# Kernel tuning notes

Measured on AMD Instinct MI355X. Metric: run time of the kernel, lower is better.

Reference implementation:

```python
import jax, jax.numpy as jnp
import numpy as np

N_NODES = 50000
N_EDGES = 800000
N_TRAIN = 40000
IN_DIM = 129  # node_dim + encoding_dim


def _gatv2(x, src, dst, Wl, Wr, att, bias, heads, out_ch, n_nodes):
    """PyG GATv2Conv (share_weights=False, concat=True, aggr='mean', eval mode).
    x: [N, F_in]; src/dst: [E]; Wl/Wr: [F_in, heads*out_ch]; att: [heads, out_ch]."""
    xl = (x @ Wl).reshape(-1, heads, out_ch)          # source transform  [N,H,C]
    xr = (x @ Wr).reshape(-1, heads, out_ch)          # target transform  [N,H,C]
    e = jax.nn.leaky_relu(xl[src] + xr[dst], 0.2)     # [E,H,C]
    logits = jnp.einsum('ehc,hc->eh', e, att)         # [E,H]
    # segment softmax over incoming edges of each target node
    m = jax.ops.segment_max(logits, dst, num_segments=n_nodes)   # [N,H]
    a = jnp.exp(logits - m[dst])
    denom = jax.ops.segment_sum(a, dst, num_segments=n_nodes)    # [N,H]
    alpha = a / denom[dst]                                       # [E,H]
    msg = xl[src] * alpha[:, :, None]                            # [E,H,C]
    summed = jax.ops.segment_sum(msg, dst, num_segments=n_nodes) # [N,H,C]
    deg = jax.ops.segment_sum(jnp.ones((src.shape[0],), x.dtype), dst,
                              num_segments=n_nodes)              # aggr='mean'
    out = summed / jnp.maximum(deg, 1.0)[:, None, None]
    return out.reshape(n_nodes, heads * out_ch) + bias


def setup_inputs() -> dict:
    key = jax.random.key(0)
    ks = jax.random.split(key, 16)
    x = jax.random.normal(ks[0], (N_NODES, IN_DIM), jnp.float32)
    edge_index = jax.random.randint(ks[1], (2, N_EDGES), 0, N_NODES, jnp.int64)
    y = jax.random.uniform(ks[2], (N_NODES,), jnp.float32)
    train_idx = jnp.sort(jax.random.randint(ks[3], (N_TRAIN,), 0, N_NODES, jnp.int64))

    def lin(k, fi, fo):
        return jax.random.normal(k, (fi, fo), jnp.float32) * (1.0 / np.sqrt(fi))

    return {
        'x': x, 'edge_index': edge_index, 'y': y, 'train_idx': train_idx,
        # layer 1: 129 -> 128, heads=2 (concat -> 256)
        'W1l': lin(ks[4], IN_DIM, 256), 'W1r': lin(ks[5], IN_DIM, 256),
        'a1': jax.random.normal(ks[6], (2, 128), jnp.float32) * 0.1,
        'b1': jnp.zeros((256,), jnp.float32),
        # layer 2: 256 -> 128, heads=1
        'W2l': lin(ks[7], 256, 128), 'W2r': lin(ks[8], 256, 128),
        'a2': jax.random.normal(ks[9], (1, 128), jnp.float32) * 0.1,
        'b2': jnp.zeros((128,), jnp.float32),
        # layer 3: 128 -> 1, heads=1
        'W3l': lin(ks[10], 128, 1), 'W3r': lin(ks[11], 128, 1),
        'a3': jax.random.normal(ks[12], (1, 1), jnp.float32) * 0.1,
        'b3': jnp.zeros((1,), jnp.float32),
    }


def reference(x, edge_index, y, train_idx,
              W1l, W1r, a1, b1, W2l, W2r, a2, b2, W3l, W3r, a3, b3):
    src, dst = edge_index[0], edge_index[1]
    n = x.shape[0]
    h = _gatv2(x, src, dst, W1l, W1r, a1, b1, 2, 128, n)   # [N,256]
    h = _gatv2(h, src, dst, W2l, W2r, a2, b2, 1, 128, n)   # [N,128]
    h = _gatv2(h, src, dst, W3l, W3r, a3, b3, 1, 1, n)     # [N,1]
    pred = jax.nn.sigmoid(h.squeeze(-1))                   # [N]
    return pred[train_idx], y[train_idx]
```

## Files before the change

### kernel.cpp

```cpp
#include <hip/hip_runtime.h>
#include <cmath>

__device__ __forceinline__ float lo16(unsigned u){ union{unsigned x; float f;} c; c.x = u << 16; return c.f; }
__device__ __forceinline__ float hi16(unsigned u){ union{unsigned x; float f;} c; c.x = u & 0xffff0000u; return c.f; }
__device__ __forceinline__ float leaky(float v){ return fmaxf(v, 0.2f*v); }
__device__ __forceinline__ unsigned short f2bf(float f){
  union { float f; unsigned u; } c; c.f = f;
  unsigned u = c.u + 0x7FFFu + ((c.u >> 16) & 1u);
  return (unsigned short)(u >> 16);
}
__device__ __forceinline__ unsigned pack2bf(float a, float b){
  return (unsigned)f2bf(a) | ((unsigned)f2bf(b) << 16);
}
__device__ __forceinline__ float mergef(float m, float M){ return (m == M) ? 1.f : __expf(m - M); }

typedef __attribute__((ext_vector_type(8))) short bfrag;
typedef __attribute__((ext_vector_type(4))) float ffrag;


__global__ void deg_kernel(const int* __restrict__ dst, int* __restrict__ degi, int E){
  int e = blockIdx.x*256 + threadIdx.x;
  if (e < E) atomicAdd(&degi[dst[e]], 1);
}

__global__ void scan_p1(const int* __restrict__ degi, int* __restrict__ bsum, int N){
  __shared__ int red[256];
  int t = threadIdx.x;
  int i = blockIdx.x*256 + t;
  red[t] = (i < N) ? degi[i] : 0;
  __syncthreads();
  for (int off = 128; off > 0; off >>= 1){
    if (t < off) red[t] += red[t + off];
    __syncthreads();
  }
  if (t == 0) bsum[blockIdx.x] = red[0];
}

__global__ void scan_p2(const int* __restrict__ bsum, int* __restrict__ boff,
                        int* __restrict__ row_off, int NB, int N){
  __shared__ int s[256];
  int t = threadIdx.x;
  int v = (t < NB) ? bsum[t] : 0;
  s[t] = v;
  __syncthreads();
  for (int off = 1; off < 256; off <<= 1){
    int q = (t >= off) ? s[t - off] : 0;
    __syncthreads();
    s[t] += q;
    __syncthreads();
  }
  if (t < NB) boff[t] = s[t] - v;
  if (t == NB-1) row_off[N] = s[t];
}

__global__ void scan_p3(const int* __restrict__ degi, const int* __restrict__ boff,
                        int* __restrict__ row_off, int N){
  __shared__ int s[256];
  int t = threadIdx.x;
  int i = blockIdx.x*256 + t;
  int v = (i < N) ? degi[i] : 0;
  s[t] = v;
  __syncthreads();
  for (int off = 1; off < 256; off <<= 1){
    int q = (t >= off) ? s[t - off] : 0;
    __syncthreads();
    s[t] += q;
    __syncthreads();
  }
  if (i < N) row_off[i] = boff[blockIdx.x] + s[t] - v;
}

__global__ void scatter_kernel(const int* __restrict__ src, const int* __restrict__ dst,
                               const int* __restrict__ row_off, int* __restrict__ cursor,
                               int* __restrict__ csr_src, int E){
  int e = blockIdx.x*256 + threadIdx.x;
  if (e < E){
    int d = dst[e];
    int pos = row_off[d] + atomicAdd(&cursor[d], 1);
    csr_src[pos] = src[e];
  }
}


__global__ void prep_all(const float* __restrict__ x,
                         const float* __restrict__ W1l, const float* __restrict__ W1r,
                         const float* __restrict__ W2l, const float* __restrict__ W2r,
                         unsigned short* __restrict__ Xbf,
                         unsigned short* __restrict__ WT1,
                         unsigned short* __restrict__ WT2, int N){
  int idx = blockIdx.x*256 + threadIdx.x;
  int n1 = N*160;
  int n2 = 2*256*160;
  int n3 = 2*128*256;
  if (idx < n1){
    int n = idx / 160, k = idx - n*160;
    Xbf[idx] = (k < 129) ? f2bf(x[(size_t)n*129 + k]) : (unsigned short)0;
  } else if (idx < n1 + n2){
    int j = idx - n1;
    int c = j / 160, k = j - c*160;
    float v = 0.f;
    if (k < 129) v = (c < 256) ? W1l[(size_t)k*256 + c] : W1r[(size_t)k*256 + (c - 256)];
    WT1[j] = f2bf(v);
  } else if (idx < n1 + n2 + n3){
    int j = idx - n1 - n2;
    int c = j >> 8, k = j & 255;
    float v = (c < 128) ? W2l[(size_t)k*128 + c] : W2r[(size_t)k*128 + (c - 128)];
    WT2[j] = f2bf(v);
  }
}


template<int CB>
__global__ __launch_bounds__(256) void gemm_dual(const unsigned short* __restrict__ Xbf,
                                                 const unsigned short* __restrict__ WT,
                                                 unsigned short* __restrict__ outL,
                                                 unsigned short* __restrict__ outR,
                                                 int N, int Kpad, int Mhalf){
  __shared__ __attribute__((aligned(16))) unsigned short Xs[128*40];
  __shared__ __attribute__((aligned(16))) unsigned short Ws[CB*128*40];
  int t = threadIdx.x;
  int n0 = blockIdx.x*128, c0 = blockIdx.y*(CB*128);
  int wv = t >> 6, lane = t & 63;
  int wr = wv >> 1, wc = wv & 1;
  int m16 = lane & 15, quad = lane >> 4;

  ffrag acc[CB][4][4];
  #pragma unroll
  for (int cb = 0; cb < CB; cb++)
    #pragma unroll
    for (int i = 0; i < 4; i++)
      #pragma unroll
      for (int j = 0; j < 4; j++) acc[cb][i][j] = (ffrag){0.f,0.f,0.f,0.f};

  for (int k0 = 0; k0 < Kpad; k0 += 32){
    uint4 zero = {0,0,0,0};
    #pragma unroll
    for (int it = 0; it < 2; it++){
      int idx = t + it*256;
      int r = idx >> 2, g = idx & 3;
      int n = n0 + r;
      uint4 v = (n < N) ? *(const uint4*)&Xbf[(size_t)n*Kpad + k0 + g*8] : zero;
      *(uint4*)&Xs[r*40 + g*8] = v;
    }
    #pragma unroll
    for (int it = 0; it < 2*CB; it++){
      int idx = t + it*256;
      int c = idx >> 2, g = idx & 3;
      uint4 v = *(const uint4*)&WT[(size_t)(c0 + c)*Kpad + k0 + g*8];
      *(uint4*)&Ws[c*40 + g*8] = v;
    }
    __syncthreads();
    bfrag a[4];
    #pragma unroll
    for (int i = 0; i < 4; i++)
      a[i] = *(const bfrag*)&Xs[(wr*64 + i*16 + m16)*40 + quad*8];
    #pragma unroll
    for (int cb = 0; cb < CB; cb++){
      bfrag b[4];
      #pragma unroll
      for (int j = 0; j < 4; j++)
        b[j] = *(const bfrag*)&Ws[(cb*128 + wc*64 + j*16 + m16)*40 + quad*8];
      #pragma unroll
      for (int i = 0; i < 4; i++)
        #pragma unroll
        for (int j = 0; j < 4; j++)
          acc[cb][i][j] = __builtin_amdgcn_mfma_f32_16x16x32_bf16(a[i], b[j], acc[cb][i][j], 0, 0, 0);
    }
    __syncthreads();
  }

  #pragma unroll
  for (int cb = 0; cb < CB; cb++){
    int gc0 = c0 + cb*128;
    bool isL = (gc0 < Mhalf);
    unsigned short* outp = isL ? outL : outR;
    int ccol0 = isL ? gc0 : (gc0 - Mhalf);
    #pragma unroll
    for (int i = 0; i < 4; i++){
      #pragma unroll
      for (int reg = 0; reg < 4; reg++){
        int rr = n0 + wr*64 + i*16 + quad*4 + reg;
        if (rr >= N) continue;
        #pragma unroll
        for (int j = 0; j < 4; j++){
          int cc = ccol0 + wc*64 + j*16 + m16;
          outp[(size_t)rr*Mhalf + cc] = f2bf(acc[cb][i][j][reg]);
        }
      }
    }
  }
}


__global__ __launch_bounds__(256) void fused_gat_wave2(
    const int* __restrict__ row_off, const int* __restrict__ csr_src,
    const unsigned short* __restrict__ xlbf, const unsigned short* __restrict__ xrbf,
    const float* __restrict__ att, const float* __restrict__ bias,
    unsigned short* __restrict__ outbf, int N)
{
  int n = blockIdx.x*4 + (threadIdx.x >> 6);
  if (n >= N) return;
  int lane = threadIdx.x & 63;
  int slot = lane >> 5;
  int sub  = lane & 31;
  int ch0  = sub*8;
  int r0 = row_off[n], r1 = row_off[n+1];
  int deg = r1 - r0;

  uint4 xru = *(const uint4*)&xrbf[(size_t)n*256 + ch0];
  float q0=lo16(xru.x), q1=hi16(xru.x), q2=lo16(xru.y), q3=hi16(xru.y);
  float q4=lo16(xru.z), q5=hi16(xru.z), q6=lo16(xru.w), q7=hi16(xru.w);
  const float4* atp = (const float4*)(att + ch0);
  float4 ata = atp[0], atb = atp[1];

  float m = -INFINITY, l = 0.f;
  float a0=0.f,a1=0.f,a2=0.f,a3=0.f,a4=0.f,a5=0.f,a6=0.f,a7=0.f;

  if (deg > 0){
    int p = r0 + slot;
    int pc = min(p, r1-1);
    uint4 cur = *(const uint4*)&xlbf[(size_t)csr_src[pc]*256 + ch0];
    for (; p < r1; p += 2){
      int pn = min(p+2, r1-1);
      uint4 nxt = *(const uint4*)&xlbf[(size_t)csr_src[pn]*256 + ch0];
      float x0=lo16(cur.x), x1=hi16(cur.x), x2=lo16(cur.y), x3=hi16(cur.y);
      float x4=lo16(cur.z), x5=hi16(cur.z), x6=lo16(cur.w), x7=hi16(cur.w);
      float dot = leaky(x0+q0)*ata.x + leaky(x1+q1)*ata.y
                + leaky(x2+q2)*ata.z + leaky(x3+q3)*ata.w
                + leaky(x4+q4)*atb.x + leaky(x5+q5)*atb.y
                + leaky(x6+q6)*atb.z + leaky(x7+q7)*atb.w;
      dot += __shfl_xor(dot, 8);
      dot += __shfl_xor(dot, 4);
      dot += __shfl_xor(dot, 2);
      dot += __shfl_xor(dot, 1);
      if (dot <= m){
        float w_ = __expf(dot - m);
        l += w_;
        a0 += w_*x0; a1 += w_*x1; a2 += w_*x2; a3 += w_*x3;
        a4 += w_*x4; a5 += w_*x5; a6 += w_*x6; a7 += w_*x7;
      } else {
        float sc = __expf(m - dot);
        l = l*sc + 1.f;
        a0 = a0*sc + x0; a1 = a1*sc + x1; a2 = a2*sc + x2; a3 = a3*sc + x3;
        a4 = a4*sc + x4; a5 = a5*sc + x5; a6 = a6*sc + x6; a7 = a7*sc + x7;
        m = dot;
      }
      cur = nxt;
    }
  }

  const float4* bvp = (const float4*)(bias + ch0);
  float4 res0 = bvp[0], res1 = bvp[1];
  if (deg > 0){
    float m2 = __shfl_xor(m, 32);
    float l2 = __shfl_xor(l, 32);
    float M  = fmaxf(m, m2);
    float fa = mergef(m, M), fb = mergef(m2, M);
    float L  = l*fa + l2*fb;
    float q;
    q = __shfl_xor(a0,32); a0 = a0*fa + q*fb;
    q = __shfl_xor(a1,32); a1 = a1*fa + q*fb;
    q = __shfl_xor(a2,32); a2 = a2*fa + q*fb;
    q = __shfl_xor(a3,32); a3 = a3*fa + q*fb;
    q = __shfl_xor(a4,32); a4 = a4*fa + q*fb;
    q = __shfl_xor(a5,32); a5 = a5*fa + q*fb;
    q = __shfl_xor(a6,32); a6 = a6*fa + q*fb;
    q = __shfl_xor(a7,32); a7 = a7*fa + q*fb;
    float inv = 1.f / (L * (float)deg);
    res0.x += a0*inv; res0.y += a1*inv; res0.z += a2*inv; res0.w += a3*inv;
    res1.x += a4*inv; res1.y += a5*inv; res1.z += a6*inv; res1.w += a7*inv;
  }
  if (slot == 0){
    uint4 u;
    u.x = pack2bf(res0.x, res0.y);
    u.y = pack2bf(res0.z, res0.w);
    u.z = pack2bf(res1.x, res1.y);
    u.w = pack2bf(res1.z, res1.w);
    *(uint4*)&outbf[(size_t)n*256 + ch0] = u;
  }
}


__global__ __launch_bounds__(256) void fused_gat_wave1(
    const int* __restrict__ row_off, const int* __restrict__ csr_src,
    const unsigned short* __restrict__ xlbf, const unsigned short* __restrict__ xrbf,
    const float* __restrict__ att, const float* __restrict__ bias,
    unsigned short* __restrict__ outbf, int N)
{
  int n = blockIdx.x*4 + (threadIdx.x >> 6);
  if (n >= N) return;
  int lane = threadIdx.x & 63;
  int slot = lane >> 4;
  int sub  = lane & 15;
  int ch0  = sub*8;
  int r0 = row_off[n], r1 = row_off[n+1];
  int deg = r1 - r0;

  uint4 xru = *(const uint4*)&xrbf[(size_t)n*128 + ch0];
  float q0=lo16(xru.x), q1=hi16(xru.x), q2=lo16(xru.y), q3=hi16(xru.y);
  float q4=lo16(xru.z), q5=hi16(xru.z), q6=lo16(xru.w), q7=hi16(xru.w);
  const float4* atp = (const float4*)(att + ch0);
  float4 ata = atp[0], atb = atp[1];

  float m = -INFINITY, l = 0.f;
  float a0=0.f,a1=0.f,a2=0.f,a3=0.f,a4=0.f,a5=0.f,a6=0.f,a7=0.f;

  if (deg > 0){
    int p = r0 + slot;
    int pc = min(p, r1-1);
    uint4 cur = *(const uint4*)&xlbf[(size_t)csr_src[pc]*128 + ch0];
    for (; p < r1; p += 4){
      int pn = min(p+4, r1-1);
      uint4 nxt = *(const uint4*)&xlbf[(size_t)csr_src[pn]*128 + ch0];
      float x0=lo16(cur.x), x1=hi16(cur.x), x2=lo16(cur.y), x3=hi16(cur.y);
      float x4=lo16(cur.z), x5=hi16(cur.z), x6=lo16(cur.w), x7=hi16(cur.w);
      float dot = leaky(x0+q0)*ata.x + leaky(x1+q1)*ata.y
                + leaky(x2+q2)*ata.z + leaky(x3+q3)*ata.w
                + leaky(x4+q4)*atb.x + leaky(x5+q5)*atb.y
                + leaky(x6+q6)*atb.z + leaky(x7+q7)*atb.w;
      dot += __shfl_xor(dot, 8);
      dot += __shfl_xor(dot, 4);
      dot += __shfl_xor(dot, 2);
      dot += __shfl_xor(dot, 1);
      if (dot <= m){
        float w_ = __expf(dot - m);
        l += w_;
        a0 += w_*x0; a1 += w_*x1; a2 += w_*x2; a3 += w_*x3;
        a4 += w_*x4; a5 += w_*x5; a6 += w_*x6; a7 += w_*x7;
      } else {
        float sc = __expf(m - dot);
        l = l*sc + 1.f;
        a0 = a0*sc + x0; a1 = a1*sc + x1; a2 = a2*sc + x2; a3 = a3*sc + x3;
        a4 = a4*sc + x4; a5 = a5*sc + x5; a6 = a6*sc + x6; a7 = a7*sc + x7;
        m = dot;
      }
      cur = nxt;
    }
  }

  const float4* bvp = (const float4*)(bias + ch0);
  float4 res0 = bvp[0], res1 = bvp[1];
  if (deg > 0){
    #pragma unroll
    for (int stage = 0; stage < 2; stage++){
      int d = 16 << stage;
      float m2 = __shfl_xor(m, d);
      float l2 = __shfl_xor(l, d);
      float M  = fmaxf(m, m2);
      float fa = mergef(m, M), fb = mergef(m2, M);
      l = l*fa + l2*fb;
      float q;
      q = __shfl_xor(a0,d); a0 = a0*fa + q*fb;
      q = __shfl_xor(a1,d); a1 = a1*fa + q*fb;
      q = __shfl_xor(a2,d); a2 = a2*fa + q*fb;
      q = __shfl_xor(a3,d); a3 = a3*fa + q*fb;
      q = __shfl_xor(a4,d); a4 = a4*fa + q*fb;
      q = __shfl_xor(a5,d); a5 = a5*fa + q*fb;
      q = __shfl_xor(a6,d); a6 = a6*fa + q*fb;
      q = __shfl_xor(a7,d); a7 = a7*fa + q*fb;
      m = M;
    }
    float inv = 1.f / (l * (float)deg);
    res0.x += a0*inv; res0.y += a1*inv; res0.z += a2*inv; res0.w += a3*inv;
    res1.x += a4*inv; res1.y += a5*inv; res1.z += a6*inv; res1.w += a7*inv;
  }
  if (slot == 0){
    uint4 u;
    u.x = pack2bf(res0.x, res0.y);
    u.y = pack2bf(res0.z, res0.w);
    u.z = pack2bf(res1.x, res1.y);
    u.w = pack2bf(res1.z, res1.w);
    *(uint4*)&outbf[(size_t)n*128 + ch0] = u;
  }
}


__global__ __launch_bounds__(256) void gemm3_kernel(const unsigned short* __restrict__ h2,
                                                    const float* __restrict__ W3l,
                                                    const float* __restrict__ W3r,
                                                    float* __restrict__ xl3,
                                                    float* __restrict__ xr3, int N){
  int n = blockIdx.x*4 + (threadIdx.x >> 6);
  int lane = threadIdx.x & 63;
  if (n >= N) return;
  unsigned u = *(const unsigned*)&h2[(size_t)n*128 + lane*2];
  float v1 = lo16(u), v2 = hi16(u);
  float al = v1*W3l[lane*2] + v2*W3l[lane*2+1];
  float ar = v1*W3r[lane*2] + v2*W3r[lane*2+1];
  #pragma unroll
  for (int off = 32; off > 0; off >>= 1){
    al += __shfl_xor(al, off);
    ar += __shfl_xor(ar, off);
  }
  if (lane == 0){ xl3[n] = al; xr3[n] = ar; }
}

__global__ __launch_bounds__(256) void aggr3_wave(
    const int* __restrict__ row_off, const int* __restrict__ csr_src,
    const float* __restrict__ xl3, const float* __restrict__ xr3,
    const float* __restrict__ a3, const float* __restrict__ b3,
    float* __restrict__ h3, int N)
{
  int n = blockIdx.x*4 + (threadIdx.x >> 6);
  if (n >= N) return;
  int lane = threadIdx.x & 63;
  int r0 = row_off[n], r1 = row_off[n+1];
  int deg = r1 - r0;
  float b = b3[0];
  if (deg == 0){ if (lane == 0) h3[n] = b; return; }
  float xrv = xr3[n];
  float aa = a3[0];
  float m = -INFINITY, den = 0.f, s = 0.f;
  for (int base = r0; base < r1; base += 64){
    int p = base + lane;
    bool valid = p < r1;
    float xlv = valid ? xl3[csr_src[p]] : 0.f;
    float t = xlv + xrv;
    float v = fmaxf(t, 0.2f*t) * aa;
    if (!valid) v = -INFINITY;
    float bm = v;
    #pragma unroll
    for (int off = 32; off > 0; off >>= 1) bm = fmaxf(bm, __shfl_xor(bm, off));
    float nm = fmaxf(m, bm);
    float a = valid ? __expf(v - nm) : 0.f;
    float bd = a, bs = a * xlv;
    #pragma unroll
    for (int off = 32; off > 0; off >>= 1){
      bd += __shfl_xor(bd, off);
      bs += __shfl_xor(bs, off);
    }
    float sc = __expf(m - nm);
    den = den*sc + bd;
    s   = s*sc + bs;
    m = nm;
  }
  if (lane == 0) h3[n] = s/den/(float)deg + b;
}

__global__ void out_kernel(const float* __restrict__ h3, const float* __restrict__ y,
                           const int* __restrict__ tidx, float* __restrict__ out, int T){
  int i = blockIdx.x*256 + threadIdx.x;
  if (i >= T) return;
  int n = tidx[i];
  out[i] = 1.f/(1.f + __expf(-h3[n]));
  out[T + i] = y[n];
}


extern "C" void kernel_launch(void* const* d_in, const int* in_sizes, int n_in,
                              void* d_out, int out_size, void* d_ws, size_t ws_size,
                              hipStream_t stream){
  const float* x    = (const float*)d_in[0];
  const int*   ei   = (const int*)d_in[1];
  const float* y    = (const float*)d_in[2];
  const int*   tidx = (const int*)d_in[3];
  const float* W1l  = (const float*)d_in[4];
  const float* W1r  = (const float*)d_in[5];
  const float* a1   = (const float*)d_in[6];
  const float* b1   = (const float*)d_in[7];
  const float* W2l  = (const float*)d_in[8];
  const float* W2r  = (const float*)d_in[9];
  const float* a2   = (const float*)d_in[10];
  const float* b2   = (const float*)d_in[11];
  const float* W3l  = (const float*)d_in[12];
  const float* W3r  = (const float*)d_in[13];
  const float* a3   = (const float*)d_in[14];
  const float* b3   = (const float*)d_in[15];

  int N = in_sizes[2];
  int E = in_sizes[1] / 2;
  int T = in_sizes[3];
  const int* src = ei;
  const int* dst = ei + E;
  int NB = (N + 255) / 256;

  char* w = (char*)d_ws;
  size_t off = 0;
  auto take = [&](size_t bytes) -> char* {
    char* p = w + off;
    off = (off + bytes + 255) & ~(size_t)255;
    return p;
  };
  int*   row_off = (int*)  take((size_t)(N+1)*4);
  int*   degi    = (int*)  take((size_t)N*4);
  int*   cursor  = (int*)  take((size_t)N*4);
  int*   bsum    = (int*)  take((size_t)NB*4);
  int*   boff    = (int*)  take((size_t)NB*4);
  int*   csr_src = (int*)  take((size_t)E*4);
  unsigned short* WT1 = (unsigned short*)take((size_t)512*160*2);
  unsigned short* WT2 = (unsigned short*)take((size_t)256*256*2);
  float* A       = (float*)take((size_t)N*256*4);
  float* B       = (float*)take((size_t)N*256*4);

  hipMemsetAsync(degi, 0, (size_t)N*4, stream);
  hipMemsetAsync(cursor, 0, (size_t)N*4, stream);
  deg_kernel<<<(E+255)/256, 256, 0, stream>>>(dst, degi, E);
  scan_p1<<<NB, 256, 0, stream>>>(degi, bsum, N);
  scan_p2<<<1, 256, 0, stream>>>(bsum, boff, row_off, NB, N);
  scan_p3<<<NB, 256, 0, stream>>>(degi, boff, row_off, N);
  scatter_kernel<<<(E+255)/256, 256, 0, stream>>>(src, dst, row_off, cursor, csr_src, E);

  unsigned short* xl1bf = (unsigned short*)A;
  unsigned short* Xbf   = (unsigned short*)(A + (size_t)N*128);
  unsigned short* h1bf  = (unsigned short*)(A + (size_t)N*128);
  unsigned short* xr1bf = (unsigned short*)B;
  float* Bu   = B + (size_t)N*128;
  float* xl3  = Bu;
  float* xr3  = Bu + N;
  float* h3   = Bu + 2*(size_t)N;

  int prep_total = N*160 + 2*256*160 + 2*128*256;
  prep_all<<<(prep_total+255)/256, 256, 0, stream>>>(x, W1l, W1r, W2l, W2r, Xbf, WT1, WT2, N);

  gemm_dual<2><<<dim3((N+127)/128, 2), 256, 0, stream>>>(Xbf, WT1, xl1bf, xr1bf, N, 160, 256);
  fused_gat_wave2<<<(N+3)/4, 256, 0, stream>>>(row_off, csr_src, xl1bf, xr1bf, a1, b1, h1bf, N);

  unsigned short* xl2bf = (unsigned short*)A;
  unsigned short* xr2bf = (unsigned short*)B;
  gemm_dual<2><<<dim3((N+127)/128, 1), 256, 0, stream>>>(h1bf, WT2, xl2bf, xr2bf, N, 256, 128);
  fused_gat_wave1<<<(N+3)/4, 256, 0, stream>>>(row_off, csr_src, xl2bf, xr2bf, a2, b2, xr2bf, N);
  unsigned short* h2bf = xr2bf;

  gemm3_kernel<<<(N+3)/4, 256, 0, stream>>>(h2bf, W3l, W3r, xl3, xr3, N);
  aggr3_wave<<<(N+3)/4, 256, 0, stream>>>(row_off, csr_src, xl3, xr3, a3, b3, h3, N);

  out_kernel<<<(T+255)/256, 256, 0, stream>>>(h3, y, tidx, (float*)d_out, T);
}
```

Baseline: 394.8 us.

## Fuse layer-3 projection into layer-2 aggregation and streamline attention math

Folds the layer-3 linear projection (gemm3) into the layer-2 fused GAT kernel, so h2 is never written out or read back. The cursor memset is dropped by having the scan seed the scatter cursors with the row offsets directly. The attention inner loops are rewritten: leaky ReLU becomes 0.6*t + 0.4*|t| with log2e pre-folded into the coefficients so exp2f replaces __expf, and the min-clamped edge prefetch is replaced by reads padded past the end of csr_src. These cut launches, memory traffic and per-edge ALU work. In exchange the prefetch reads one row beyond each node's range and relies on four padding entries at the end of csr_src.

New measurement: 419.8 us. +6.3%, slower.

```diff
diff --git a/kernel.cpp b/kernel.cpp
--- a/kernel.cpp
+++ b/kernel.cpp
@@ -3,7 +3,6 @@
 
 __device__ __forceinline__ float lo16(unsigned u){ union{unsigned x; float f;} c; c.x = u << 16; return c.f; }
 __device__ __forceinline__ float hi16(unsigned u){ union{unsigned x; float f;} c; c.x = u & 0xffff0000u; return c.f; }
-__device__ __forceinline__ float leaky(float v){ return fmaxf(v, 0.2f*v); }
 __device__ __forceinline__ unsigned short f2bf(float f){
   union { float f; unsigned u; } c; c.f = f;
   unsigned u = c.u + 0x7FFFu + ((c.u >> 16) & 1u);
@@ -12,7 +11,9 @@
 __device__ __forceinline__ unsigned pack2bf(float a, float b){
   return (unsigned)f2bf(a) | ((unsigned)f2bf(b) << 16);
 }
-__device__ __forceinline__ float mergef(float m, float M){ return (m == M) ? 1.f : __expf(m - M); }
+__device__ __forceinline__ float mergef2(float m, float M){ return (m == M) ? 1.f : exp2f(m - M); }
+
+#define LOG2E 1.4426950408889634f
 
 typedef __attribute__((ext_vector_type(8))) short bfrag;
 typedef __attribute__((ext_vector_type(4))) float ffrag;
@@ -54,7 +55,7 @@
 }
 
 __global__ void scan_p3(const int* __restrict__ degi, const int* __restrict__ boff,
-                        int* __restrict__ row_off, int N){
+                        int* __restrict__ row_off, int* __restrict__ cur, int N){
   __shared__ int s[256];
   int t = threadIdx.x;
   int i = blockIdx.x*256 + t;
@@ -67,17 +68,21 @@
     s[t] += q;
     __syncthreads();
   }
-  if (i < N) row_off[i] = boff[blockIdx.x] + s[t] - v;
+  if (i < N){
+    int ro = boff[blockIdx.x] + s[t] - v;
+    row_off[i] = ro;
+    cur[i] = ro;
+  }
 }
 
 __global__ void scatter_kernel(const int* __restrict__ src, const int* __restrict__ dst,
-                               const int* __restrict__ row_off, int* __restrict__ cursor,
-                               int* __restrict__ csr_src, int E){
+                               int* __restrict__ cur, int* __restrict__ csr_src, int E){
   int e = blockIdx.x*256 + threadIdx.x;
   if (e < E){
-    int d = dst[e];
-    int pos = row_off[d] + atomicAdd(&cursor[d], 1);
+    int pos = atomicAdd(&cur[dst[e]], 1);
     csr_src[pos] = src[e];
+  } else if (e < E + 4){
+    csr_src[e] = 0;
   }
 }
 
@@ -211,52 +216,60 @@
   float q0=lo16(xru.x), q1=hi16(xru.x), q2=lo16(xru.y), q3=hi16(xru.y);
   float q4=lo16(xru.z), q5=hi16(xru.z), q6=lo16(xru.w), q7=hi16(xru.w);
   const float4* atp = (const float4*)(att + ch0);
-  float4 ata = atp[0], atb = atp[1];
+  float4 aa = atp[0], ab = atp[1];
+  float4 p6a, p6b, p4a, p4b;
+  p6a.x=0.6f*LOG2E*aa.x; p6a.y=0.6f*LOG2E*aa.y; p6a.z=0.6f*LOG2E*aa.z; p6a.w=0.6f*LOG2E*aa.w;
+  p6b.x=0.6f*LOG2E*ab.x; p6b.y=0.6f*LOG2E*ab.y; p6b.z=0.6f*LOG2E*ab.z; p6b.w=0.6f*LOG2E*ab.w;
+  p4a.x=0.4f*LOG2E*aa.x; p4a.y=0.4f*LOG2E*aa.y; p4a.z=0.4f*LOG2E*aa.z; p4a.w=0.4f*LOG2E*aa.w;
+  p4b.x=0.4f*LOG2E*ab.x; p4b.y=0.4f*LOG2E*ab.y; p4b.z=0.4f*LOG2E*ab.z; p4b.w=0.4f*LOG2E*ab.w;
 
   float m = -INFINITY, l = 0.f;
   float a0=0.f,a1=0.f,a2=0.f,a3=0.f,a4=0.f,a5=0.f,a6=0.f,a7=0.f;
 
-  if (deg > 0){
-    int p = r0 + slot;
-    int pc = min(p, r1-1);
-    uint4 cur = *(const uint4*)&xlbf[(size_t)csr_src[pc]*256 + ch0];
-    for (; p < r1; p += 2){
-      int pn = min(p+2, r1-1);
-      uint4 nxt = *(const uint4*)&xlbf[(size_t)csr_src[pn]*256 + ch0];
-      float x0=lo16(cur.x), x1=hi16(cur.x), x2=lo16(cur.y), x3=hi16(cur.y);
-      float x4=lo16(cur.z), x5=hi16(cur.z), x6=lo16(cur.w), x7=hi16(cur.w);
-      float dot = leaky(x0+q0)*ata.x + leaky(x1+q1)*ata.y
-                + leaky(x2+q2)*ata.z + leaky(x3+q3)*ata.w
-                + leaky(x4+q4)*atb.x + leaky(x5+q5)*atb.y
-                + leaky(x6+q6)*atb.z + leaky(x7+q7)*atb.w;
-      dot += __shfl_xor(dot, 8);
-      dot += __shfl_xor(dot, 4);
-      dot += __shfl_xor(dot, 2);
-      dot += __shfl_xor(dot, 1);
-      if (dot <= m){
-        float w_ = __expf(dot - m);
-        l += w_;
-        a0 += w_*x0; a1 += w_*x1; a2 += w_*x2; a3 += w_*x3;
-        a4 += w_*x4; a5 += w_*x5; a6 += w_*x6; a7 += w_*x7;
-      } else {
-        float sc = __expf(m - dot);
-        l = l*sc + 1.f;
-        a0 = a0*sc + x0; a1 = a1*sc + x1; a2 = a2*sc + x2; a3 = a3*sc + x3;
-        a4 = a4*sc + x4; a5 = a5*sc + x5; a6 = a6*sc + x6; a7 = a7*sc + x7;
-        m = dot;
-      }
-      cur = nxt;
-    }
-  }
-
-  const float4* bvp = (const float4*)(bias + ch0);
-  float4 res0 = bvp[0], res1 = bvp[1];
-  if (deg > 0){
+  const char* xlb = (const char*)xlbf;
+  unsigned chb = (unsigned)ch0*2;
+  int p = r0 + slot;
+  unsigned off0 = ((unsigned)csr_src[p] << 9) + chb;
+  uint4 cur = *(const uint4*)(xlb + off0);
+  for (; p < r1; p += 2){
+    unsigned offn = ((unsigned)csr_src[p+2] << 9) + chb;
+    uint4 nxt = *(const uint4*)(xlb + offn);
+    float x0=lo16(cur.x), x1=hi16(cur.x), x2=lo16(cur.y), x3=hi16(cur.y);
+    float x4=lo16(cur.z), x5=hi16(cur.z), x6=lo16(cur.w), x7=hi16(cur.w);
+    float t0=x0+q0, t1=x1+q1, t2=x2+q2, t3=x3+q3;
+    float t4=x4+q4, t5=x5+q5, t6=x6+q6, t7=x7+q7;
+    float s6 = p6a.x*t0;
+    s6 = fmaf(p6a.y,t1,s6); s6 = fmaf(p6a.z,t2,s6); s6 = fmaf(p6a.w,t3,s6);
+    s6 = fmaf(p6b.x,t4,s6); s6 = fmaf(p6b.y,t5,s6); s6 = fmaf(p6b.z,t6,s6); s6 = fmaf(p6b.w,t7,s6);
+    float s4 = p4a.x*fabsf(t0);
+    s4 = fmaf(p4a.y,fabsf(t1),s4); s4 = fmaf(p4a.z,fabsf(t2),s4); s4 = fmaf(p4a.w,fabsf(t3),s4);
+    s4 = fmaf(p4b.x,fabsf(t4),s4); s4 = fmaf(p4b.y,fabsf(t5),s4); s4 = fmaf(p4b.z,fabsf(t6),s4); s4 = fmaf(p4b.w,fabsf(t7),s4);
+    float dot = s6 + s4;
+    dot += __shfl_xor(dot, 8);
+    dot += __shfl_xor(dot, 4);
+    dot += __shfl_xor(dot, 2);
+    dot += __shfl_xor(dot, 1);
+    if (dot <= m){
+      float w_ = exp2f(dot - m);
+      l += w_;
+      a0 += w_*x0; a1 += w_*x1; a2 += w_*x2; a3 += w_*x3;
+      a4 += w_*x4; a5 += w_*x5; a6 += w_*x6; a7 += w_*x7;
+    } else {
+      float sc = exp2f(m - dot);
+      l = l*sc + 1.f;
+      a0 = a0*sc + x0; a1 = a1*sc + x1; a2 = a2*sc + x2; a3 = a3*sc + x3;
+      a4 = a4*sc + x4; a5 = a5*sc + x5; a6 = a6*sc + x6; a7 = a7*sc + x7;
+      m = dot;
+    }
+    cur = nxt;
+  }
+
+  {
     float m2 = __shfl_xor(m, 32);
     float l2 = __shfl_xor(l, 32);
     float M  = fmaxf(m, m2);
-    float fa = mergef(m, M), fb = mergef(m2, M);
-    float L  = l*fa + l2*fb;
+    float fa = mergef2(m, M), fb = mergef2(m2, M);
+    l = l*fa + l2*fb;
     float q;
     q = __shfl_xor(a0,32); a0 = a0*fa + q*fb;
     q = __shfl_xor(a1,32); a1 = a1*fa + q*fb;
@@ -266,10 +279,12 @@
     q = __shfl_xor(a5,32); a5 = a5*fa + q*fb;
     q = __shfl_xor(a6,32); a6 = a6*fa + q*fb;
     q = __shfl_xor(a7,32); a7 = a7*fa + q*fb;
-    float inv = 1.f / (L * (float)deg);
-    res0.x += a0*inv; res0.y += a1*inv; res0.z += a2*inv; res0.w += a3*inv;
-    res1.x += a4*inv; res1.y += a5*inv; res1.z += a6*inv; res1.w += a7*inv;
-  }
+  }
+  float inv = (deg > 0) ? 1.f/(l*(float)deg) : 0.f;
+  const float4* bvp = (const float4*)(bias + ch0);
+  float4 res0 = bvp[0], res1 = bvp[1];
+  res0.x += a0*inv; res0.y += a1*inv; res0.z += a2*inv; res0.w += a3*inv;
+  res1.x += a4*inv; res1.y += a5*inv; res1.z += a6*inv; res1.w += a7*inv;
   if (slot == 0){
     uint4 u;
     u.x = pack2bf(res0.x, res0.y);
@@ -285,13 +300,14 @@
     const int* __restrict__ row_off, const int* __restrict__ csr_src,
     const unsigned short* __restrict__ xlbf, const unsigned short* __restrict__ xrbf,
     const float* __restrict__ att, const float* __restrict__ bias,
-    unsigned short* __restrict__ outbf, int N)
+    const float* __restrict__ W3l, const float* __restrict__ W3r,
+    float* __restrict__ xl3, float* __restrict__ xr3, int N)
 {
   int n = blockIdx.x*4 + (threadIdx.x >> 6);
   if (n >= N) return;
   int lane = threadIdx.x & 63;
+  int sub  = lane & 15;
   int slot = lane >> 4;
-  int sub  = lane & 15;
   int ch0  = sub*8;
   int r0 = row_off[n], r1 = row_off[n+1];
   int deg = r1 - r0;
@@ -300,100 +316,92 @@
   float q0=lo16(xru.x), q1=hi16(xru.x), q2=lo16(xru.y), q3=hi16(xru.y);
   float q4=lo16(xru.z), q5=hi16(xru.z), q6=lo16(xru.w), q7=hi16(xru.w);
   const float4* atp = (const float4*)(att + ch0);
-  float4 ata = atp[0], atb = atp[1];
+  float4 aa = atp[0], ab = atp[1];
+  float4 p6a, p6b, p4a, p4b;
+  p6a.x=0.6f*LOG2E*aa.x; p6a.y=0.6f*LOG2E*aa.y; p6a.z=0.6f*LOG2E*aa.z; p6a.w=0.6f*LOG2E*aa.w;
+  p6b.x=0.6f*LOG2E*ab.x; p6b.y=0.6f*LOG2E*ab.y; p6b.z=0.6f*LOG2E*ab.z; p6b.w=0.6f*LOG2E*ab.w;
+  p4a.x=0.4f*LOG2E*aa.x; p4a.y=0.4f*LOG2E*aa.y; p4a.z=0.4f*LOG2E*aa.z; p4a.w=0.4f*LOG2E*aa.w;
+  p4b.x=0.4f*LOG2E*ab.x; p4b.y=0.4f*LOG2E*ab.y; p4b.z=0.4f*LOG2E*ab.z; p4b.w=0.4f*LOG2E*ab.w;
 
   float m = -INFINITY, l = 0.f;
   float a0=0.f,a1=0.f,a2=0.f,a3=0.f,a4=0.f,a5=0.f,a6=0.f,a7=0.f;
 
-  if (deg > 0){
-    int p = r0 + slot;
-    int pc = min(p, r1-1);
-    uint4 cur = *(const uint4*)&xlbf[(size_t)csr_src[pc]*128 + ch0];
-    for (; p < r1; p += 4){
-      int pn = min(p+4, r1-1);
-      uint4 nxt = *(const uint4*)&xlbf[(size_t)csr_src[pn]*128 + ch0];
-      float x0=lo16(cur.x), x1=hi16(cur.x), x2=lo16(cur.y), x3=hi16(cur.y);
-      float x4=lo16(cur.z), x5=hi16(cur.z), x6=lo16(cur.w), x7=hi16(cur.w);
-      float dot = leaky(x0+q0)*ata.x + leaky(x1+q1)*ata.y
-                + leaky(x2+q2)*ata.z + leaky(x3+q3)*ata.w
-                + leaky(x4+q4)*atb.x + leaky(x5+q5)*atb.y
-                + leaky(x6+q6)*atb.z + leaky(x7+q7)*atb.w;
-      dot += __shfl_xor(dot, 8);
-      dot += __shfl_xor(dot, 4);
-      dot += __shfl_xor(dot, 2);
-      dot += __shfl_xor(dot, 1);
-      if (dot <= m){
-        float w_ = __expf(dot - m);
-        l += w_;
-        a0 += w_*x0; a1 += w_*x1; a2 += w_*x2; a3 += w_*x3;
-        a4 += w_*x4; a5 += w_*x5; a6 += w_*x6; a7 += w_*x7;
-      } else {
-        float sc = __expf(m - dot);
-        l = l*sc + 1.f;
-        a0 = a0*sc + x0; a1 = a1*sc + x1; a2 = a2*sc + x2; a3 = a3*sc + x3;
-        a4 = a4*sc + x4; a5 = a5*sc + x5; a6 = a6*sc + x6; a7 = a7*sc + x7;
-        m = dot;
-      }
-      cur = nxt;
-    }
-  }
-
+  const char* xlb = (const char*)xlbf;
+  unsigned chb = (unsigned)ch0*2;
+  int p = r0 + slot;
+  unsigned off0 = ((unsigned)csr_src[p] << 8) + chb;
+  uint4 cur = *(const uint4*)(xlb + off0);
+  for (; p < r1; p += 4){
+    unsigned offn = ((unsigned)csr_src[p+4] << 8) + chb;
+    uint4 nxt = *(const uint4*)(xlb + offn);
+    float x0=lo16(cur.x), x1=hi16(cur.x), x2=lo16(cur.y), x3=hi16(cur.y);
+    float x4=lo16(cur.z), x5=hi16(cur.z), x6=lo16(cur.w), x7=hi16(cur.w);
+    float t0=x0+q0, t1=x1+q1, t2=x2+q2, t3=x3+q3;
+    float t4=x4+q4, t5=x5+q5, t6=x6+q6, t7=x7+q7;
+    float s6 = p6a.x*t0;
+    s6 = fmaf(p6a.y,t1,s6); s6 = fmaf(p6a.z,t2,s6); s6 = fmaf(p6a.w,t3,s6);
+    s6 = fmaf(p6b.x,t4,s6); s6 = fmaf(p6b.y,t5,s6); s6 = fmaf(p6b.z,t6,s6); s6 = fmaf(p6b.w,t7,s6);
+    float s4 = p4a.x*fabsf(t0);
+    s4 = fmaf(p4a.y,fabsf(t1),s4); s4 = fmaf(p4a.z,fabsf(t2),s4); s4 = fmaf(p4a.w,fabsf(t3),s4);
+    s4 = fmaf(p4b.x,fabsf(t4),s4); s4 = fmaf(p4b.y,fabsf(t5),s4); s4 = fmaf(p4b.z,fabsf(t6),s4); s4 = fmaf(p4b.w,fabsf(t7),s4);
+    float dot = s6 + s4;
+    dot += __shfl_xor(dot, 8);
+    dot += __shfl_xor(dot, 4);
+    dot += __shfl_xor(dot, 2);
+    dot += __shfl_xor(dot, 1);
+    if (dot <= m){
+      float w_ = exp2f(dot - m);
+      l += w_;
+      a0 += w_*x0; a1 += w_*x1; a2 += w_*x2; a3 += w_*x3;
+      a4 += w_*x4; a5 += w_*x5; a6 += w_*x6; a7 += w_*x7;
+    } else {
+      float sc = exp2f(m - dot);
+      l = l*sc + 1.f;
+      a0 = a0*sc + x0; a1 = a1*sc + x1; a2 = a2*sc + x2; a3 = a3*sc + x3;
+      a4 = a4*sc + x4; a5 = a5*sc + x5; a6 = a6*sc + x6; a7 = a7*sc + x7;
+      m = dot;
+    }
+    cur = nxt;
+  }
+
+  #pragma unroll
+  for (int stage = 0; stage < 2; stage++){
+    int d = 16 << stage;
+    float m2 = __shfl_xor(m, d);
+    float l2 = __shfl_xor(l, d);
+    float M  = fmaxf(m, m2);
+    float fa = mergef2(m, M), fb = mergef2(m2, M);
+    l = l*fa + l2*fb;
+    float q;
+    q = __shfl_xor(a0,d); a0 = a0*fa + q*fb;
+    q = __shfl_xor(a1,d); a1 = a1*fa + q*fb;
+    q = __shfl_xor(a2,d); a2 = a2*fa + q*fb;
+    q = __shfl_xor(a3,d); a3 = a3*fa + q*fb;
+    q = __shfl_xor(a4,d); a4 = a4*fa + q*fb;
+    q = __shfl_xor(a5,d); a5 = a5*fa + q*fb;
+    q = __shfl_xor(a6,d); a6 = a6*fa + q*fb;
+    q = __shfl_xor(a7,d); a7 = a7*fa + q*fb;
+    m = M;
+  }
+  float inv = (deg > 0) ? 1.f/(l*(float)deg) : 0.f;
   const float4* bvp = (const float4*)(bias + ch0);
   float4 res0 = bvp[0], res1 = bvp[1];
-  if (deg > 0){
-    #pragma unroll
-    for (int stage = 0; stage < 2; stage++){
-      int d = 16 << stage;
-      float m2 = __shfl_xor(m, d);
-      float l2 = __shfl_xor(l, d);
-      float M  = fmaxf(m, m2);
-      float fa = mergef(m, M), fb = mergef(m2, M);
-      l = l*fa + l2*fb;
-      float q;
-      q = __shfl_xor(a0,d); a0 = a0*fa + q*fb;
-      q = __shfl_xor(a1,d); a1 = a1*fa + q*fb;
-      q = __shfl_xor(a2,d); a2 = a2*fa + q*fb;
-      q = __shfl_xor(a3,d); a3 = a3*fa + q*fb;
-      q = __shfl_xor(a4,d); a4 = a4*fa + q*fb;
-      q = __shfl_xor(a5,d); a5 = a5*fa + q*fb;
-      q = __shfl_xor(a6,d); a6 = a6*fa + q*fb;
-      q = __shfl_xor(a7,d); a7 = a7*fa + q*fb;
-      m = M;
-    }
-    float inv = 1.f / (l * (float)deg);
-    res0.x += a0*inv; res0.y += a1*inv; res0.z += a2*inv; res0.w += a3*inv;
-    res1.x += a4*inv; res1.y += a5*inv; res1.z += a6*inv; res1.w += a7*inv;
-  }
-  if (slot == 0){
-    uint4 u;
-    u.x = pack2bf(res0.x, res0.y);
-    u.y = pack2bf(res0.z, res0.w);
-    u.z = pack2bf(res1.x, res1.y);
-    u.w = pack2bf(res1.z, res1.w);
-    *(uint4*)&outbf[(size_t)n*128 + ch0] = u;
-  }
-}
-
-
-__global__ __launch_bounds__(256) void gemm3_kernel(const unsigned short* __restrict__ h2,
-                                                    const float* __restrict__ W3l,
-                                                    const float* __restrict__ W3r,
-                                                    float* __restrict__ xl3,
-                                                    float* __restrict__ xr3, int N){
-  int n = blockIdx.x*4 + (threadIdx.x >> 6);
-  int lane = threadIdx.x & 63;
-  if (n >= N) return;
-  unsigned u = *(const unsigned*)&h2[(size_t)n*128 + lane*2];
-  float v1 = lo16(u), v2 = hi16(u);
-  float al = v1*W3l[lane*2] + v2*W3l[lane*2+1];
-  float ar = v1*W3r[lane*2] + v2*W3r[lane*2+1];
-  #pragma unroll
-  for (int off = 32; off > 0; off >>= 1){
-    al += __shfl_xor(al, off);
-    ar += __shfl_xor(ar, off);
-  }
-  if (lane == 0){ xl3[n] = al; xr3[n] = ar; }
-}
+  res0.x += a0*inv; res0.y += a1*inv; res0.z += a2*inv; res0.w += a3*inv;
+  res1.x += a4*inv; res1.y += a5*inv; res1.z += a6*inv; res1.w += a7*inv;
+
+  float4 wla = *(const float4*)(W3l + ch0);
+  float4 wlb = *(const float4*)(W3l + ch0 + 4);
+  float4 wra = *(const float4*)(W3r + ch0);
+  float4 wrb = *(const float4*)(W3r + ch0 + 4);
+  float sl = res0.x*wla.x + res0.y*wla.y + res0.z*wla.z + res0.w*wla.w
+           + res1.x*wlb.x + res1.y*wlb.y + res1.z*wlb.z + res1.w*wlb.w;
+  float sr = res0.x*wra.x + res0.y*wra.y + res0.z*wra.z + res0.w*wra.w
+           + res1.x*wrb.x + res1.y*wrb.y + res1.z*wrb.z + res1.w*wrb.w;
+  sl += __shfl_xor(sl, 8); sl += __shfl_xor(sl, 4); sl += __shfl_xor(sl, 2); sl += __shfl_xor(sl, 1);
+  sr += __shfl_xor(sr, 8); sr += __shfl_xor(sr, 4); sr += __shfl_xor(sr, 2); sr += __shfl_xor(sr, 1);
+  if (lane == 0){ xl3[n] = sl; xr3[n] = sr; }
+}
+
 
 __global__ __launch_bounds__(256) void aggr3_wave(
     const int* __restrict__ row_off, const int* __restrict__ csr_src,
@@ -409,7 +417,7 @@
   float b = b3[0];
   if (deg == 0){ if (lane == 0) h3[n] = b; return; }
   float xrv = xr3[n];
-  float aa = a3[0];
+  float aa = a3[0] * LOG2E;
   float m = -INFINITY, den = 0.f, s = 0.f;
   for (int base = r0; base < r1; base += 64){
     int p = base + lane;
@@ -422,14 +430,14 @@
     #pragma unroll
     for (int off = 32; off > 0; off >>= 1) bm = fmaxf(bm, __shfl_xor(bm, off));
     float nm = fmaxf(m, bm);
-    float a = valid ? __expf(v - nm) : 0.f;
+    float a = valid ? exp2f(v - nm) : 0.f;
     float bd = a, bs = a * xlv;
     #pragma unroll
     for (int off = 32; off > 0; off >>= 1){
       bd += __shfl_xor(bd, off);
       bs += __shfl_xor(bs, off);
     }
-    float sc = __expf(m - nm);
+    float sc = exp2f(m - nm);
     den = den*sc + bd;
     s   = s*sc + bs;
     m = nm;
@@ -483,22 +491,21 @@
   };
   int*   row_off = (int*)  take((size_t)(N+1)*4);
   int*   degi    = (int*)  take((size_t)N*4);
-  int*   cursor  = (int*)  take((size_t)N*4);
+  int*   cur     = (int*)  take((size_t)N*4);
   int*   bsum    = (int*)  take((size_t)NB*4);
   int*   boff    = (int*)  take((size_t)NB*4);
-  int*   csr_src = (int*)  take((size_t)E*4);
+  int*   csr_src = (int*)  take((size_t)(E+4)*4);
   unsigned short* WT1 = (unsigned short*)take((size_t)512*160*2);
   unsigned short* WT2 = (unsigned short*)take((size_t)256*256*2);
   float* A       = (float*)take((size_t)N*256*4);
   float* B       = (float*)take((size_t)N*256*4);
 
   hipMemsetAsync(degi, 0, (size_t)N*4, stream);
-  hipMemsetAsync(cursor, 0, (size_t)N*4, stream);
   deg_kernel<<<(E+255)/256, 256, 0, stream>>>(dst, degi, E);
   scan_p1<<<NB, 256, 0, stream>>>(degi, bsum, N);
   scan_p2<<<1, 256, 0, stream>>>(bsum, boff, row_off, NB, N);
-  scan_p3<<<NB, 256, 0, stream>>>(degi, boff, row_off, N);
-  scatter_kernel<<<(E+255)/256, 256, 0, stream>>>(src, dst, row_off, cursor, csr_src, E);
+  scan_p3<<<NB, 256, 0, stream>>>(degi, boff, row_off, cur, N);
+  scatter_kernel<<<(E+4+255)/256, 256, 0, stream>>>(src, dst, cur, csr_src, E);
 
   unsigned short* xl1bf = (unsigned short*)A;
   unsigned short* Xbf   = (unsigned short*)(A + (size_t)N*128);
@@ -518,10 +525,9 @@
   unsigned short* xl2bf = (unsigned short*)A;
   unsigned short* xr2bf = (unsigned short*)B;
   gemm_dual<2><<<dim3((N+127)/128, 1), 256, 0, stream>>>(h1bf, WT2, xl2bf, xr2bf, N, 256, 128);
-  fused_gat_wave1<<<(N+3)/4, 256, 0, stream>>>(row_off, csr_src, xl2bf, xr2bf, a2, b2, xr2bf, N);
-  unsigned short* h2bf = xr2bf;
-
-  gemm3_kernel<<<(N+3)/4, 256, 0, stream>>>(h2bf, W3l, W3r, xl3, xr3, N);
+  fused_gat_wave1<<<(N+3)/4, 256, 0, stream>>>(row_off, csr_src, xl2bf, xr2bf, a2, b2,
+                                               W3l, W3r, xl3, xr3, N);
+
   aggr3_wave<<<(N+3)/4, 256, 0, stream>>>(row_off, csr_src, xl3, xr3, a3, b3, h3, N);
 
   out_kernel<<<(T+255)/256, 256, 0, stream>>>(h3, y, tidx, (float*)d_out, T);
```
